# Optimization experiments

Hardware: AMD Instinct MI355X
Metric: run time of the kernel (lower is better)

## Reference

```python
import jax, jax.numpy as jnp
import numpy as np

N = 10000       # n_nodes
E = 640000      # n_edges (avg degree 64)
D_IN = 128      # in_feats
D_H = 128       # n_hidden
N_CLS = 64      # n_classes


def setup_inputs() -> dict:
    key = jax.random.key(0)
    k1, k2, k3, k4, k5, k6 = jax.random.split(key, 6)
    features = jax.random.normal(k1, (N, D_IN), dtype=jnp.float32)
    src = jax.random.randint(k2, (E,), 0, N, dtype=jnp.int32)
    dst = jax.random.randint(k3, (E,), 0, N, dtype=jnp.int32)
    s = 0.05  # small init scale to keep activations bounded across 3 layers
    # Stored as [in, out]; equivalent to torch Linear weight [out, in] transposed.
    W0 = jax.random.normal(k4, (D_IN, D_H), dtype=jnp.float32) * s
    W1 = jax.random.normal(k5, (D_H, D_H), dtype=jnp.float32) * s
    W2 = jax.random.normal(k6, (D_H, N_CLS), dtype=jnp.float32) * s
    return {"features": features, "W0": W0, "W1": W1, "W2": W2,
            "src": src, "dst": dst}


def reference(features, W0, W1, W2, src, dst):
    # GINConv with aggregator 'sum', eps=0 (learn_eps=False):
    #   h' = Linear(h + sum_{(u->v) in E} h[u] scattered to v)
    # Dropout is identity at inference; 'activation' is unused in the module.
    def gin_layer(h, W):
        agg = jax.ops.segment_sum(h[src], dst, num_segments=N)  # [N, d]
        return (h + agg) @ W

    h = gin_layer(features, W0)
    h = gin_layer(h, W1)
    h = gin_layer(h, W2)
    return h
```

## Files before the change

kernel.cpp:

```cpp
#include <hip/hip_runtime.h>
#include <hip/hip_bf16.h>

#define NN 10000
#define NE 640000
#define D_IN 128
#define D_H 128
#define N_CLS 64
#define CAP 160
#define GRP 157
#define CAPC 4800
#define CCS 16
#define SENT 10000
#define EPB 1024
#define AB 625
#define W01B 16
#define WPB 4

__device__ __forceinline__ float blo(unsigned u) { return __uint_as_float(u << 16); }
__device__ __forceinline__ float bhi(unsigned u) { return __uint_as_float(u & 0xffff0000u); }
__device__ __forceinline__ unsigned short f2bf(float f) {
    unsigned u = __float_as_uint(f);
    return (unsigned short)((u + 0x7fffu + ((u >> 16) & 1u)) >> 16);
}
__device__ __forceinline__ unsigned packbf(float a, float b) {
    return (unsigned)f2bf(a) | ((unsigned)f2bf(b) << 16);
}

__global__ __launch_bounds__(256) void prep_a(const int* __restrict__ src,
                                              const int* __restrict__ dst,
                                              int* __restrict__ coarse_cnt,
                                              unsigned* __restrict__ coarse,
                                              const float* __restrict__ W0,
                                              const float* __restrict__ W1,
                                              float* __restrict__ W01) {
    int bid = blockIdx.x;
    if (bid >= AB) {
        int t = (bid - AB) * 256 + threadIdx.x;
        int i = t >> 5;
        int jb = (t & 31) << 2;
        float c0 = 0.f, c1 = 0.f, c2 = 0.f, c3 = 0.f;
        for (int k = 0; k < 128; ++k) {
            float a = W0[i * 128 + k];
            float4 b = *(const float4*)&W1[k * 128 + jb];
            c0 += a * b.x; c1 += a * b.y; c2 += a * b.z; c3 += a * b.w;
        }
        *(float4*)&W01[i * 128 + jb] = make_float4(c0, c1, c2, c3);
        return;
    }
    __shared__ unsigned stage[EPB];
    __shared__ int hist[GRP], gbase[GRP], cur[GRP];
    const int t = threadIdx.x;
    for (int i = t; i < GRP; i += 256) hist[i] = 0;
    __syncthreads();
    const int e0 = bid * EPB;
    for (int i = t; i < EPB; i += 256) {
        int s = src[e0 + i];
        int d = dst[e0 + i];
        stage[i] = (unsigned)s | ((unsigned)d << 16);
        atomicAdd(&hist[d >> 6], 1);
    }
    __syncthreads();
    for (int i = t; i < GRP; i += 256) {
        gbase[i] = atomicAdd(&coarse_cnt[i * CCS], hist[i]);
        cur[i] = 0;
    }
    __syncthreads();
    for (int i = t; i < EPB; i += 256) {
        unsigned u = stage[i];
        int g = u >> 22;
        int r = atomicAdd(&cur[g], 1);
        coarse[g * CAPC + gbase[g] + r] = u;
    }
}

__global__ __launch_bounds__(1024) void prep_b(const int* __restrict__ coarse_cnt,
                                               const unsigned* __restrict__ coarse,
                                               int* __restrict__ cnt,
                                               unsigned short* __restrict__ colbuf,
                                               const float* __restrict__ W01,
                                               const float* __restrict__ W2,
                                               unsigned* __restrict__ wbp) {
    const int g = blockIdx.x;
    const int t = threadIdx.x;
    if (g >= GRP) {
        int s = (g - GRP) * 1024 + t;
        int kp = s >> 6, j = s & 63;
        float c0 = 0.f, c1 = 0.f;
        const float* r0 = W01 + (2 * kp) * 128;
        const float* r1 = r0 + 128;
        for (int k = 0; k < 128; ++k) {
            float w2 = W2[k * 64 + j];
            c0 += r0[k] * w2;
            c1 += r1[k] * w2;
        }
        wbp[kp * 64 + j] = packbf(c0, c1);
        return;
    }
    __shared__ int cur[64];
    __shared__ unsigned short sbuf[64][CAP];
    if (t < 64) cur[t] = 0;
    __syncthreads();
    const int m = coarse_cnt[g * CCS];
    const unsigned* cb = coarse + g * CAPC;
    for (int i = t; i < m; i += 1024) {
        unsigned u = cb[i];
        int s = (int)(u & 0xFFFFu);
        int dl = (int)(u >> 16) - (g << 6);
        int r = atomicAdd(&cur[dl], 1);
        sbuf[dl][r] = (unsigned short)s;
    }
    __syncthreads();
    if (t < 64) {
        int n = (g << 6) + t;
        if (n < NN) {
            int c = cur[t];
            int pad = (32 - (c & 31)) & 31;
            for (int k = 0; k < pad; ++k) sbuf[t][c + k] = (unsigned short)SENT;
            cnt[n] = c + pad;
        }
    }
    __syncthreads();
    const uint4* s4 = (const uint4*)sbuf;
    for (int idx = t; idx < 64 * (CAP / 8); idx += 1024) {
        int node = (g << 6) + (idx / (CAP / 8));
        if (node < NN)
            ((uint4*)colbuf)[(size_t)node * (CAP / 8) + (idx % (CAP / 8))] = s4[idx];
    }
}

__global__ __launch_bounds__(256, 4) void gemm0(const float* __restrict__ feat,
                                                const unsigned* __restrict__ Wbp,
                                                unsigned short* __restrict__ g0) {
    __shared__ float xs[4][128];
    const int tid = threadIdx.x;
    const int wave = tid >> 6;
    const int lane = tid & 63;
    const int n = blockIdx.x * 4 + wave;
    float2 f = *(const float2*)&feat[(size_t)n * 128 + lane * 2];
    xs[wave][lane * 2]     = f.x;
    xs[wave][lane * 2 + 1] = f.y;
    __syncthreads();
    const int j = lane;
    float acc = 0.f;
    for (int k = 0; k < 128; k += 4) {
        unsigned wp0 = Wbp[(k >> 1) * 64 + j];
        unsigned wp1 = Wbp[((k >> 1) + 1) * 64 + j];
        float4 xv = *(const float4*)&xs[wave][k];
        acc += xv.x * blo(wp0) + xv.y * bhi(wp0) + xv.z * blo(wp1) + xv.w * bhi(wp1);
    }
    g0[(size_t)n * 64 + j] = f2bf(acc);
    if (blockIdx.x == 0 && tid < 16) {
        ((uint2*)(g0 + (size_t)SENT * 64))[tid] = make_uint2(0u, 0u);
    }
}

__global__ __launch_bounds__(256, 4) void agg64b(const uint4* __restrict__ tb4,
                                                 const int* __restrict__ cnt,
                                                 const unsigned short* __restrict__ colbuf,
                                                 unsigned short* __restrict__ tb2) {
    constexpr int M = 4;
    const int base = blockIdx.x * M;
    const int tid = threadIdx.x;
    const int wave = tid >> 6;
    const int lane = tid & 63;
    const int sub = lane >> 3;
    const int off = lane & 7;

    const int n = __builtin_amdgcn_readfirstlane(base + wave);
    float a0, a1, a2, a3, a4, a5, a6, a7;
    if (sub == 0) {
        uint4 u = tb4[n * 8 + off];
        a0 = blo(u.x); a1 = bhi(u.x); a2 = blo(u.y); a3 = bhi(u.y);
        a4 = blo(u.z); a5 = bhi(u.z); a6 = blo(u.w); a7 = bhi(u.w);
    } else {
        a0 = a1 = a2 = a3 = a4 = a5 = a6 = a7 = 0.f;
    }
    const int NCH = __builtin_amdgcn_readfirstlane(cnt[n]) >> 5;
    const uint2* cl = (const uint2*)(colbuf + n * CAP);
    const int hi4 = sub >> 2;
    const int wsel = (sub >> 1) & 1;
    const int sh = (sub & 1) << 4;
    uint2 p0 = cl[0], p1 = cl[1], p2 = cl[2], p3 = cl[3];
    uint2 p4 = cl[4], p5 = cl[5], p6 = cl[6], p7 = cl[7];
    for (int c = 0; c < NCH; ++c) {
        unsigned q0 = hi4 ? (wsel ? p1.y : p1.x) : (wsel ? p0.y : p0.x);
        unsigned q1 = hi4 ? (wsel ? p3.y : p3.x) : (wsel ? p2.y : p2.x);
        unsigned q2 = hi4 ? (wsel ? p5.y : p5.x) : (wsel ? p4.y : p4.x);
        unsigned q3 = hi4 ? (wsel ? p7.y : p7.x) : (wsel ? p6.y : p6.x);
        int s0 = (int)((q0 >> sh) & 0xffffu);
        int s1 = (int)((q1 >> sh) & 0xffffu);
        int s2 = (int)((q2 >> sh) & 0xffffu);
        int s3 = (int)((q3 >> sh) & 0xffffu);
        uint4 u0 = tb4[s0 * 8 + off];
        uint4 u1 = tb4[s1 * 8 + off];
        uint4 u2 = tb4[s2 * 8 + off];
        uint4 u3 = tb4[s3 * 8 + off];
        {
            const uint2* nx = cl + 8 * (c + 1);
            p0 = nx[0]; p1 = nx[1]; p2 = nx[2]; p3 = nx[3];
            p4 = nx[4]; p5 = nx[5]; p6 = nx[6]; p7 = nx[7];
        }
        a0 += (blo(u0.x) + blo(u1.x)) + (blo(u2.x) + blo(u3.x));
        a1 += (bhi(u0.x) + bhi(u1.x)) + (bhi(u2.x) + bhi(u3.x));
        a2 += (blo(u0.y) + blo(u1.y)) + (blo(u2.y) + blo(u3.y));
        a3 += (bhi(u0.y) + bhi(u1.y)) + (bhi(u2.y) + bhi(u3.y));
        a4 += (blo(u0.z) + blo(u1.z)) + (blo(u2.z) + blo(u3.z));
        a5 += (bhi(u0.z) + bhi(u1.z)) + (bhi(u2.z) + bhi(u3.z));
        a6 += (blo(u0.w) + blo(u1.w)) + (blo(u2.w) + blo(u3.w));
        a7 += (bhi(u0.w) + bhi(u1.w)) + (bhi(u2.w) + bhi(u3.w));
    }
    a0 += __shfl_xor(a0, 8); a0 += __shfl_xor(a0, 16); a0 += __shfl_xor(a0, 32);
    a1 += __shfl_xor(a1, 8); a1 += __shfl_xor(a1, 16); a1 += __shfl_xor(a1, 32);
    a2 += __shfl_xor(a2, 8); a2 += __shfl_xor(a2, 16); a2 += __shfl_xor(a2, 32);
    a3 += __shfl_xor(a3, 8); a3 += __shfl_xor(a3, 16); a3 += __shfl_xor(a3, 32);
    a4 += __shfl_xor(a4, 8); a4 += __shfl_xor(a4, 16); a4 += __shfl_xor(a4, 32);
    a5 += __shfl_xor(a5, 8); a5 += __shfl_xor(a5, 16); a5 += __shfl_xor(a5, 32);
    a6 += __shfl_xor(a6, 8); a6 += __shfl_xor(a6, 16); a6 += __shfl_xor(a6, 32);
    a7 += __shfl_xor(a7, 8); a7 += __shfl_xor(a7, 16); a7 += __shfl_xor(a7, 32);
    if (sub == 0) {
        unsigned short* o = tb2 + (size_t)n * 64 + 8 * off;
        *(uint4*)o = make_uint4(packbf(a0, a1), packbf(a2, a3),
                                packbf(a4, a5), packbf(a6, a7));
    }
    if (blockIdx.x == 0 && tid < 16) {
        ((uint2*)(tb2 + (size_t)SENT * 64))[tid] = make_uint2(0u, 0u);
    }
}

__global__ __launch_bounds__(256, 4) void agg64f(const uint4* __restrict__ tb4,
                                                 const int* __restrict__ cnt,
                                                 const unsigned short* __restrict__ colbuf,
                                                 float* __restrict__ outf) {
    constexpr int M = 4;
    const int base = blockIdx.x * M;
    const int tid = threadIdx.x;
    const int wave = tid >> 6;
    const int lane = tid & 63;
    const int sub = lane >> 3;
    const int off = lane & 7;

    const int n = __builtin_amdgcn_readfirstlane(base + wave);
    float a0, a1, a2, a3, a4, a5, a6, a7;
    if (sub == 0) {
        uint4 u = tb4[n * 8 + off];
        a0 = blo(u.x); a1 = bhi(u.x); a2 = blo(u.y); a3 = bhi(u.y);
        a4 = blo(u.z); a5 = bhi(u.z); a6 = blo(u.w); a7 = bhi(u.w);
    } else {
        a0 = a1 = a2 = a3 = a4 = a5 = a6 = a7 = 0.f;
    }
    const int NCH = __builtin_amdgcn_readfirstlane(cnt[n]) >> 5;
    const uint2* cl = (const uint2*)(colbuf + n * CAP);
    const int hi4 = sub >> 2;
    const int wsel = (sub >> 1) & 1;
    const int sh = (sub & 1) << 4;
    uint2 p0 = cl[0], p1 = cl[1], p2 = cl[2], p3 = cl[3];
    uint2 p4 = cl[4], p5 = cl[5], p6 = cl[6], p7 = cl[7];
    for (int c = 0; c < NCH; ++c) {
        unsigned q0 = hi4 ? (wsel ? p1.y : p1.x) : (wsel ? p0.y : p0.x);
        unsigned q1 = hi4 ? (wsel ? p3.y : p3.x) : (wsel ? p2.y : p2.x);
        unsigned q2 = hi4 ? (wsel ? p5.y : p5.x) : (wsel ? p4.y : p4.x);
        unsigned q3 = hi4 ? (wsel ? p7.y : p7.x) : (wsel ? p6.y : p6.x);
        int s0 = (int)((q0 >> sh) & 0xffffu);
        int s1 = (int)((q1 >> sh) & 0xffffu);
        int s2 = (int)((q2 >> sh) & 0xffffu);
        int s3 = (int)((q3 >> sh) & 0xffffu);
        uint4 u0 = tb4[s0 * 8 + off];
        uint4 u1 = tb4[s1 * 8 + off];
        uint4 u2 = tb4[s2 * 8 + off];
        uint4 u3 = tb4[s3 * 8 + off];
        {
            const uint2* nx = cl + 8 * (c + 1);
            p0 = nx[0]; p1 = nx[1]; p2 = nx[2]; p3 = nx[3];
            p4 = nx[4]; p5 = nx[5]; p6 = nx[6]; p7 = nx[7];
        }
        a0 += (blo(u0.x) + blo(u1.x)) + (blo(u2.x) + blo(u3.x));
        a1 += (bhi(u0.x) + bhi(u1.x)) + (bhi(u2.x) + bhi(u3.x));
        a2 += (blo(u0.y) + blo(u1.y)) + (blo(u2.y) + blo(u3.y));
        a3 += (bhi(u0.y) + bhi(u1.y)) + (bhi(u2.y) + bhi(u3.y));
        a4 += (blo(u0.z) + blo(u1.z)) + (blo(u2.z) + blo(u3.z));
        a5 += (bhi(u0.z) + bhi(u1.z)) + (bhi(u2.z) + bhi(u3.z));
        a6 += (blo(u0.w) + blo(u1.w)) + (blo(u2.w) + blo(u3.w));
        a7 += (bhi(u0.w) + bhi(u1.w)) + (bhi(u2.w) + bhi(u3.w));
    }
    a0 += __shfl_xor(a0, 8); a0 += __shfl_xor(a0, 16); a0 += __shfl_xor(a0, 32);
    a1 += __shfl_xor(a1, 8); a1 += __shfl_xor(a1, 16); a1 += __shfl_xor(a1, 32);
    a2 += __shfl_xor(a2, 8); a2 += __shfl_xor(a2, 16); a2 += __shfl_xor(a2, 32);
    a3 += __shfl_xor(a3, 8); a3 += __shfl_xor(a3, 16); a3 += __shfl_xor(a3, 32);
    a4 += __shfl_xor(a4, 8); a4 += __shfl_xor(a4, 16); a4 += __shfl_xor(a4, 32);
    a5 += __shfl_xor(a5, 8); a5 += __shfl_xor(a5, 16); a5 += __shfl_xor(a5, 32);
    a6 += __shfl_xor(a6, 8); a6 += __shfl_xor(a6, 16); a6 += __shfl_xor(a6, 32);
    a7 += __shfl_xor(a7, 8); a7 += __shfl_xor(a7, 16); a7 += __shfl_xor(a7, 32);
    if (sub == 0) {
        float* o = outf + (size_t)n * N_CLS + 8 * off;
        *(float4*)o       = make_float4(a0, a1, a2, a3);
        *(float4*)(o + 4) = make_float4(a4, a5, a6, a7);
    }
}

extern "C" void kernel_launch(void* const* d_in, const int* in_sizes, int n_in,
                              void* d_out, int out_size, void* d_ws, size_t ws_size,
                              hipStream_t stream) {
    const float* feat = (const float*)d_in[0];
    const float* W0   = (const float*)d_in[1];
    const float* W1   = (const float*)d_in[2];
    const float* W2   = (const float*)d_in[3];
    const int*   src  = (const int*)d_in[4];
    const int*   dst  = (const int*)d_in[5];
    float* out = (float*)d_out;

    int* coarse_cnt        = (int*)d_ws;
    int* cnt               = coarse_cnt + GRP * CCS;
    unsigned short* colbuf = (unsigned short*)(cnt + NN + 8);
    unsigned* coarse       = (unsigned*)(colbuf + (size_t)NN * CAP);
    unsigned* g0u          = coarse + (size_t)GRP * CAPC;
    unsigned* tbu          = g0u + (size_t)(NN + 1) * 32;
    unsigned* tb2u         = tbu + (size_t)(NN + 1) * 32;
    float* W01             = (float*)(tb2u + (size_t)(NN + 1) * 32);
    unsigned* wbp          = (unsigned*)(W01 + 16384);
    unsigned short* g0     = (unsigned short*)g0u;
    unsigned short* tb     = (unsigned short*)tbu;
    unsigned short* tb2    = (unsigned short*)tb2u;

    hipMemsetAsync(coarse_cnt, 0, GRP * CCS * sizeof(int), stream);
    prep_a<<<AB + W01B, 256, 0, stream>>>(src, dst, coarse_cnt, coarse, W0, W1, W01);
    prep_b<<<GRP + WPB, 1024, 0, stream>>>(coarse_cnt, coarse, cnt, colbuf,
                                           W01, W2, wbp);

    gemm0<<<NN / 4, 256, 0, stream>>>(feat, wbp, g0);
    agg64b<<<NN / 4, 256, 0, stream>>>((const uint4*)g0, cnt, colbuf, tb);
    agg64b<<<NN / 4, 256, 0, stream>>>((const uint4*)tb, cnt, colbuf, tb2);
    agg64f<<<NN / 4, 256, 0, stream>>>((const uint4*)tb2, cnt, colbuf, out);
}
```

Measured before the change: 137.2 us.

## Build CSR adjacency with direct global atomics instead of two-level bucketing

Replaces the two-pass coarse-bucket then shared-memory fine-sort construction of per-node neighbor lists with a single pass that does global atomicAdd on per-node counters and scatters 16-bit source indices directly into colbuf, followed by a light padding kernel. This removes the intermediate coarse buffer and a large shared-memory kernel, but adds 640k contended global atomics and scattered 2-byte writes. It also makes neighbor order within a row nondeterministic, which changes the floating-point summation order.

```diff
diff --git a/kernel.cpp b/kernel.cpp
--- a/kernel.cpp
+++ b/kernel.cpp
@@ -7,14 +7,11 @@
 #define D_H 128
 #define N_CLS 64
 #define CAP 160
-#define GRP 157
-#define CAPC 4800
-#define CCS 16
 #define SENT 10000
-#define EPB 1024
-#define AB 625
+#define EB 625
 #define W01B 16
-#define WPB 4
+#define PB 40
+#define WPB 16
 
 __device__ __forceinline__ float blo(unsigned u) { return __uint_as_float(u << 16); }
 __device__ __forceinline__ float bhi(unsigned u) { return __uint_as_float(u & 0xffff0000u); }
@@ -26,16 +23,16 @@
     return (unsigned)f2bf(a) | ((unsigned)f2bf(b) << 16);
 }
 
-__global__ __launch_bounds__(256) void prep_a(const int* __restrict__ src,
-                                              const int* __restrict__ dst,
-                                              int* __restrict__ coarse_cnt,
-                                              unsigned* __restrict__ coarse,
-                                              const float* __restrict__ W0,
-                                              const float* __restrict__ W1,
-                                              float* __restrict__ W01) {
+__global__ __launch_bounds__(256) void prep1(const int* __restrict__ src,
+                                             const int* __restrict__ dst,
+                                             int* __restrict__ cnt,
+                                             unsigned short* __restrict__ colbuf,
+                                             const float* __restrict__ W0,
+                                             const float* __restrict__ W1,
+                                             float* __restrict__ W01) {
     int bid = blockIdx.x;
-    if (bid >= AB) {
-        int t = (bid - AB) * 256 + threadIdx.x;
+    if (bid >= EB) {
+        int t = (bid - EB) * 256 + threadIdx.x;
         int i = t >> 5;
         int jb = (t & 31) << 2;
         float c0 = 0.f, c1 = 0.f, c2 = 0.f, c3 = 0.f;
@@ -47,43 +44,24 @@
         *(float4*)&W01[i * 128 + jb] = make_float4(c0, c1, c2, c3);
         return;
     }
-    __shared__ unsigned stage[EPB];
-    __shared__ int hist[GRP], gbase[GRP], cur[GRP];
-    const int t = threadIdx.x;
-    for (int i = t; i < GRP; i += 256) hist[i] = 0;
-    __syncthreads();
-    const int e0 = bid * EPB;
-    for (int i = t; i < EPB; i += 256) {
-        int s = src[e0 + i];
-        int d = dst[e0 + i];
-        stage[i] = (unsigned)s | ((unsigned)d << 16);
-        atomicAdd(&hist[d >> 6], 1);
-    }
-    __syncthreads();
-    for (int i = t; i < GRP; i += 256) {
-        gbase[i] = atomicAdd(&coarse_cnt[i * CCS], hist[i]);
-        cur[i] = 0;
-    }
-    __syncthreads();
-    for (int i = t; i < EPB; i += 256) {
-        unsigned u = stage[i];
-        int g = u >> 22;
-        int r = atomicAdd(&cur[g], 1);
-        coarse[g * CAPC + gbase[g] + r] = u;
-    }
-}
-
-__global__ __launch_bounds__(1024) void prep_b(const int* __restrict__ coarse_cnt,
-                                               const unsigned* __restrict__ coarse,
-                                               int* __restrict__ cnt,
-                                               unsigned short* __restrict__ colbuf,
-                                               const float* __restrict__ W01,
-                                               const float* __restrict__ W2,
-                                               unsigned* __restrict__ wbp) {
-    const int g = blockIdx.x;
-    const int t = threadIdx.x;
-    if (g >= GRP) {
-        int s = (g - GRP) * 1024 + t;
+    int t = bid * 256 + threadIdx.x;
+    int4 s4 = ((const int4*)src)[t];
+    int4 d4 = ((const int4*)dst)[t];
+    int r;
+    r = atomicAdd(&cnt[d4.x], 1); colbuf[(size_t)d4.x * CAP + r] = (unsigned short)s4.x;
+    r = atomicAdd(&cnt[d4.y], 1); colbuf[(size_t)d4.y * CAP + r] = (unsigned short)s4.y;
+    r = atomicAdd(&cnt[d4.z], 1); colbuf[(size_t)d4.z * CAP + r] = (unsigned short)s4.z;
+    r = atomicAdd(&cnt[d4.w], 1); colbuf[(size_t)d4.w * CAP + r] = (unsigned short)s4.w;
+}
+
+__global__ __launch_bounds__(256) void prep2(int* __restrict__ cnt,
+                                             unsigned short* __restrict__ colbuf,
+                                             const float* __restrict__ W01,
+                                             const float* __restrict__ W2,
+                                             unsigned* __restrict__ wbp) {
+    int bid = blockIdx.x;
+    if (bid >= PB) {
+        int s = (bid - PB) * 256 + threadIdx.x;
         int kp = s >> 6, j = s & 63;
         float c0 = 0.f, c1 = 0.f;
         const float* r0 = W01 + (2 * kp) * 128;
@@ -96,35 +74,13 @@
         wbp[kp * 64 + j] = packbf(c0, c1);
         return;
     }
-    __shared__ int cur[64];
-    __shared__ unsigned short sbuf[64][CAP];
-    if (t < 64) cur[t] = 0;
-    __syncthreads();
-    const int m = coarse_cnt[g * CCS];
-    const unsigned* cb = coarse + g * CAPC;
-    for (int i = t; i < m; i += 1024) {
-        unsigned u = cb[i];
-        int s = (int)(u & 0xFFFFu);
-        int dl = (int)(u >> 16) - (g << 6);
-        int r = atomicAdd(&cur[dl], 1);
-        sbuf[dl][r] = (unsigned short)s;
-    }
-    __syncthreads();
-    if (t < 64) {
-        int n = (g << 6) + t;
-        if (n < NN) {
-            int c = cur[t];
-            int pad = (32 - (c & 31)) & 31;
-            for (int k = 0; k < pad; ++k) sbuf[t][c + k] = (unsigned short)SENT;
-            cnt[n] = c + pad;
-        }
-    }
-    __syncthreads();
-    const uint4* s4 = (const uint4*)sbuf;
-    for (int idx = t; idx < 64 * (CAP / 8); idx += 1024) {
-        int node = (g << 6) + (idx / (CAP / 8));
-        if (node < NN)
-            ((uint4*)colbuf)[(size_t)node * (CAP / 8) + (idx % (CAP / 8))] = s4[idx];
+    int n = bid * 256 + threadIdx.x;
+    if (n < NN) {
+        int c = cnt[n];
+        int pad = (32 - (c & 31)) & 31;
+        unsigned short* b = colbuf + (size_t)n * CAP;
+        for (int k = 0; k < pad; ++k) b[c + k] = (unsigned short)SENT;
+        cnt[n] = c + pad;
     }
 }
 
@@ -176,7 +132,7 @@
         a0 = a1 = a2 = a3 = a4 = a5 = a6 = a7 = 0.f;
     }
     const int NCH = __builtin_amdgcn_readfirstlane(cnt[n]) >> 5;
-    const uint2* cl = (const uint2*)(colbuf + n * CAP);
+    const uint2* cl = (const uint2*)(colbuf + (size_t)n * CAP);
     const int hi4 = sub >> 2;
     const int wsel = (sub >> 1) & 1;
     const int sh = (sub & 1) << 4;
@@ -249,7 +205,7 @@
         a0 = a1 = a2 = a3 = a4 = a5 = a6 = a7 = 0.f;
     }
     const int NCH = __builtin_amdgcn_readfirstlane(cnt[n]) >> 5;
-    const uint2* cl = (const uint2*)(colbuf + n * CAP);
+    const uint2* cl = (const uint2*)(colbuf + (size_t)n * CAP);
     const int hi4 = sub >> 2;
     const int wsel = (sub >> 1) & 1;
     const int sh = (sub & 1) << 4;
@@ -308,11 +264,9 @@
     const int*   dst  = (const int*)d_in[5];
     float* out = (float*)d_out;
 
-    int* coarse_cnt        = (int*)d_ws;
-    int* cnt               = coarse_cnt + GRP * CCS;
-    unsigned short* colbuf = (unsigned short*)(cnt + NN + 8);
-    unsigned* coarse       = (unsigned*)(colbuf + (size_t)NN * CAP);
-    unsigned* g0u          = coarse + (size_t)GRP * CAPC;
+    int* cnt               = (int*)d_ws;
+    unsigned short* colbuf = (unsigned short*)(cnt + NN + 32);
+    unsigned* g0u          = (unsigned*)(colbuf + (size_t)NN * CAP + 64);
     unsigned* tbu          = g0u + (size_t)(NN + 1) * 32;
     unsigned* tb2u         = tbu + (size_t)(NN + 1) * 32;
     float* W01             = (float*)(tb2u + (size_t)(NN + 1) * 32);
@@ -321,10 +275,9 @@
     unsigned short* tb     = (unsigned short*)tbu;
     unsigned short* tb2    = (unsigned short*)tb2u;
 
-    hipMemsetAsync(coarse_cnt, 0, GRP * CCS * sizeof(int), stream);
-    prep_a<<<AB + W01B, 256, 0, stream>>>(src, dst, coarse_cnt, coarse, W0, W1, W01);
-    prep_b<<<GRP + WPB, 1024, 0, stream>>>(coarse_cnt, coarse, cnt, colbuf,
-                                           W01, W2, wbp);
+    (void)hipMemsetAsync(cnt, 0, NN * sizeof(int), stream);
+    prep1<<<EB + W01B, 256, 0, stream>>>(src, dst, cnt, colbuf, W0, W1, W01);
+    prep2<<<PB + WPB, 256, 0, stream>>>(cnt, colbuf, W01, W2, wbp);
 
     gemm0<<<NN / 4, 256, 0, stream>>>(feat, wbp, g0);
     agg64b<<<NN / 4, 256, 0, stream>>>((const uint4*)g0, cnt, colbuf, tb);
```

Result: slower. 152.9 us (+11.4%).

## Fuse gemm and three aggregation passes into one cooperative persistent kernel

Applied to the files above, without the earlier changes.

Replaces the four separate launches (gemm0 and three aggregation passes) with a single cooperative kernel on a fixed grid of 1024 blocks. Each block loops over node blocks and uses grid-wide syncs between stages. The aim is to remove kernel launch gaps and tail effects between dependent stages. In exchange it adds grid barrier cost and ties concurrency to the fixed grid size. It falls back to the old launches if the cooperative launch fails.

```diff
diff --git a/kernel.cpp b/kernel.cpp
--- a/kernel.cpp
+++ b/kernel.cpp
@@ -1,5 +1,8 @@
 #include <hip/hip_runtime.h>
 #include <hip/hip_bf16.h>
+#include <hip/hip_cooperative_groups.h>
+
+namespace cg = cooperative_groups;
 
 #define NN 10000
 #define NE 640000
@@ -15,6 +18,8 @@
 #define AB 625
 #define W01B 16
 #define WPB 4
+#define CGRID 1024
+#define NBLK (NN / 4)
 
 __device__ __forceinline__ float blo(unsigned u) { return __uint_as_float(u << 16); }
 __device__ __forceinline__ float bhi(unsigned u) { return __uint_as_float(u & 0xffff0000u); }
@@ -128,55 +133,44 @@
     }
 }
 
-__global__ __launch_bounds__(256, 4) void gemm0(const float* __restrict__ feat,
-                                                const unsigned* __restrict__ Wbp,
-                                                unsigned short* __restrict__ g0) {
-    __shared__ float xs[4][128];
-    const int tid = threadIdx.x;
-    const int wave = tid >> 6;
-    const int lane = tid & 63;
-    const int n = blockIdx.x * 4 + wave;
+__device__ __forceinline__ void gemm0_step(const float* __restrict__ feat,
+                                           const unsigned* __restrict__ Wbp,
+                                           unsigned short* __restrict__ g0,
+                                           float xsrow[128],
+                                           int n, int lane) {
     float2 f = *(const float2*)&feat[(size_t)n * 128 + lane * 2];
-    xs[wave][lane * 2]     = f.x;
-    xs[wave][lane * 2 + 1] = f.y;
-    __syncthreads();
-    const int j = lane;
+    xsrow[lane * 2]     = f.x;
+    xsrow[lane * 2 + 1] = f.y;
     float acc = 0.f;
     for (int k = 0; k < 128; k += 4) {
-        unsigned wp0 = Wbp[(k >> 1) * 64 + j];
-        unsigned wp1 = Wbp[((k >> 1) + 1) * 64 + j];
-        float4 xv = *(const float4*)&xs[wave][k];
+        unsigned wp0 = Wbp[(k >> 1) * 64 + lane];
+        unsigned wp1 = Wbp[((k >> 1) + 1) * 64 + lane];
+        float4 xv = *(const float4*)&xsrow[k];
         acc += xv.x * blo(wp0) + xv.y * bhi(wp0) + xv.z * blo(wp1) + xv.w * bhi(wp1);
     }
-    g0[(size_t)n * 64 + j] = f2bf(acc);
-    if (blockIdx.x == 0 && tid < 16) {
-        ((uint2*)(g0 + (size_t)SENT * 64))[tid] = make_uint2(0u, 0u);
-    }
-}
-
-__global__ __launch_bounds__(256, 4) void agg64b(const uint4* __restrict__ tb4,
-                                                 const int* __restrict__ cnt,
-                                                 const unsigned short* __restrict__ colbuf,
-                                                 unsigned short* __restrict__ tb2) {
-    constexpr int M = 4;
-    const int base = blockIdx.x * M;
-    const int tid = threadIdx.x;
-    const int wave = tid >> 6;
-    const int lane = tid & 63;
+    g0[(size_t)n * 64 + lane] = f2bf(acc);
+}
+
+template <bool LAST>
+__device__ __forceinline__ void agg_step(const uint4* __restrict__ in4,
+                                         const int* __restrict__ cnt,
+                                         const unsigned short* __restrict__ colbuf,
+                                         unsigned short* __restrict__ outb,
+                                         float* __restrict__ outf,
+                                         int blk, int wave, int lane) {
     const int sub = lane >> 3;
     const int off = lane & 7;
-
-    const int n = __builtin_amdgcn_readfirstlane(base + wave);
+    const int n = __builtin_amdgcn_readfirstlane(blk * 4 + wave);
     float a0, a1, a2, a3, a4, a5, a6, a7;
     if (sub == 0) {
-        uint4 u = tb4[n * 8 + off];
+        uint4 u = in4[n * 8 + off];
         a0 = blo(u.x); a1 = bhi(u.x); a2 = blo(u.y); a3 = bhi(u.y);
         a4 = blo(u.z); a5 = bhi(u.z); a6 = blo(u.w); a7 = bhi(u.w);
     } else {
         a0 = a1 = a2 = a3 = a4 = a5 = a6 = a7 = 0.f;
     }
     const int NCH = __builtin_amdgcn_readfirstlane(cnt[n]) >> 5;
-    const uint2* cl = (const uint2*)(colbuf + n * CAP);
+    const uint2* cl = (const uint2*)(colbuf + (size_t)n * CAP);
     const int hi4 = sub >> 2;
     const int wsel = (sub >> 1) & 1;
     const int sh = (sub & 1) << 4;
@@ -191,10 +185,10 @@
         int s1 = (int)((q1 >> sh) & 0xffffu);
         int s2 = (int)((q2 >> sh) & 0xffffu);
         int s3 = (int)((q3 >> sh) & 0xffffu);
-        uint4 u0 = tb4[s0 * 8 + off];
-        uint4 u1 = tb4[s1 * 8 + off];
-        uint4 u2 = tb4[s2 * 8 + off];
-        uint4 u3 = tb4[s3 * 8 + off];
+        uint4 u0 = in4[s0 * 8 + off];
+        uint4 u1 = in4[s1 * 8 + off];
+        uint4 u2 = in4[s2 * 8 + off];
+        uint4 u3 = in4[s3 * 8 + off];
         {
             const uint2* nx = cl + 8 * (c + 1);
             p0 = nx[0]; p1 = nx[1]; p2 = nx[2]; p3 = nx[3];
@@ -218,10 +212,37 @@
     a6 += __shfl_xor(a6, 8); a6 += __shfl_xor(a6, 16); a6 += __shfl_xor(a6, 32);
     a7 += __shfl_xor(a7, 8); a7 += __shfl_xor(a7, 16); a7 += __shfl_xor(a7, 32);
     if (sub == 0) {
-        unsigned short* o = tb2 + (size_t)n * 64 + 8 * off;
-        *(uint4*)o = make_uint4(packbf(a0, a1), packbf(a2, a3),
-                                packbf(a4, a5), packbf(a6, a7));
-    }
+        if (LAST) {
+            float* o = outf + (size_t)n * N_CLS + 8 * off;
+            *(float4*)o       = make_float4(a0, a1, a2, a3);
+            *(float4*)(o + 4) = make_float4(a4, a5, a6, a7);
+        } else {
+            unsigned short* o = outb + (size_t)n * 64 + 8 * off;
+            *(uint4*)o = make_uint4(packbf(a0, a1), packbf(a2, a3),
+                                    packbf(a4, a5), packbf(a6, a7));
+        }
+    }
+}
+
+__global__ __launch_bounds__(256, 4) void gemm0(const float* __restrict__ feat,
+                                                const unsigned* __restrict__ Wbp,
+                                                unsigned short* __restrict__ g0) {
+    __shared__ float xs[4][128];
+    const int tid = threadIdx.x;
+    const int wave = tid >> 6;
+    const int lane = tid & 63;
+    gemm0_step(feat, Wbp, g0, xs[wave], blockIdx.x * 4 + wave, lane);
+    if (blockIdx.x == 0 && tid < 16) {
+        ((uint2*)(g0 + (size_t)SENT * 64))[tid] = make_uint2(0u, 0u);
+    }
+}
+
+__global__ __launch_bounds__(256, 4) void agg64b(const uint4* __restrict__ tb4,
+                                                 const int* __restrict__ cnt,
+                                                 const unsigned short* __restrict__ colbuf,
+                                                 unsigned short* __restrict__ tb2) {
+    const int tid = threadIdx.x;
+    agg_step<false>(tb4, cnt, colbuf, tb2, nullptr, blockIdx.x, tid >> 6, tid & 63);
     if (blockIdx.x == 0 && tid < 16) {
         ((uint2*)(tb2 + (size_t)SENT * 64))[tid] = make_uint2(0u, 0u);
     }
@@ -231,70 +252,44 @@
                                                  const int* __restrict__ cnt,
                                                  const unsigned short* __restrict__ colbuf,
                                                  float* __restrict__ outf) {
-    constexpr int M = 4;
-    const int base = blockIdx.x * M;
+    const int tid = threadIdx.x;
+    agg_step<true>(tb4, cnt, colbuf, nullptr, outf, blockIdx.x, tid >> 6, tid & 63);
+}
+
+__global__ __launch_bounds__(256, 4) void mega(const float* __restrict__ feat,
+                                               const unsigned* __restrict__ Wbp,
+                                               unsigned short* __restrict__ g0,
+                                               const int* __restrict__ cnt,
+                                               const unsigned short* __restrict__ colbuf,
+                                               unsigned short* __restrict__ tb,
+                                               unsigned short* __restrict__ tb2,
+                                               float* __restrict__ outf) {
+    cg::grid_group grid = cg::this_grid();
+    __shared__ float xs[4][128];
     const int tid = threadIdx.x;
     const int wave = tid >> 6;
     const int lane = tid & 63;
-    const int sub = lane >> 3;
-    const int off = lane & 7;
-
-    const int n = __builtin_amdgcn_readfirstlane(base + wave);
-    float a0, a1, a2, a3, a4, a5, a6, a7;
-    if (sub == 0) {
-        uint4 u = tb4[n * 8 + off];
-        a0 = blo(u.x); a1 = bhi(u.x); a2 = blo(u.y); a3 = bhi(u.y);
-        a4 = blo(u.z); a5 = bhi(u.z); a6 = blo(u.w); a7 = bhi(u.w);
-    } else {
-        a0 = a1 = a2 = a3 = a4 = a5 = a6 = a7 = 0.f;
-    }
-    const int NCH = __builtin_amdgcn_readfirstlane(cnt[n]) >> 5;
-    const uint2* cl = (const uint2*)(colbuf + n * CAP);
-    const int hi4 = sub >> 2;
-    const int wsel = (sub >> 1) & 1;
-    const int sh = (sub & 1) << 4;
-    uint2 p0 = cl[0], p1 = cl[1], p2 = cl[2], p3 = cl[3];
-    uint2 p4 = cl[4], p5 = cl[5], p6 = cl[6], p7 = cl[7];
-    for (int c = 0; c < NCH; ++c) {
-        unsigned q0 = hi4 ? (wsel ? p1.y : p1.x) : (wsel ? p0.y : p0.x);
-        unsigned q1 = hi4 ? (wsel ? p3.y : p3.x) : (wsel ? p2.y : p2.x);
-        unsigned q2 = hi4 ? (wsel ? p5.y : p5.x) : (wsel ? p4.y : p4.x);
-        unsigned q3 = hi4 ? (wsel ? p7.y : p7.x) : (wsel ? p6.y : p6.x);
-        int s0 = (int)((q0 >> sh) & 0xffffu);
-        int s1 = (int)((q1 >> sh) & 0xffffu);
-        int s2 = (int)((q2 >> sh) & 0xffffu);
-        int s3 = (int)((q3 >> sh) & 0xffffu);
-        uint4 u0 = tb4[s0 * 8 + off];
-        uint4 u1 = tb4[s1 * 8 + off];
-        uint4 u2 = tb4[s2 * 8 + off];
-        uint4 u3 = tb4[s3 * 8 + off];
-        {
-            const uint2* nx = cl + 8 * (c + 1);
-            p0 = nx[0]; p1 = nx[1]; p2 = nx[2]; p3 = nx[3];
-            p4 = nx[4]; p5 = nx[5]; p6 = nx[6]; p7 = nx[7];
-        }
-        a0 += (blo(u0.x) + blo(u1.x)) + (blo(u2.x) + blo(u3.x));
-        a1 += (bhi(u0.x) + bhi(u1.x)) + (bhi(u2.x) + bhi(u3.x));
-        a2 += (blo(u0.y) + blo(u1.y)) + (blo(u2.y) + blo(u3.y));
-        a3 += (bhi(u0.y) + bhi(u1.y)) + (bhi(u2.y) + bhi(u3.y));
-        a4 += (blo(u0.z) + blo(u1.z)) + (blo(u2.z) + blo(u3.z));
-        a5 += (bhi(u0.z) + bhi(u1.z)) + (bhi(u2.z) + bhi(u3.z));
-        a6 += (blo(u0.w) + blo(u1.w)) + (blo(u2.w) + blo(u3.w));
-        a7 += (bhi(u0.w) + bhi(u1.w)) + (bhi(u2.w) + bhi(u3.w));
-    }
-    a0 += __shfl_xor(a0, 8); a0 += __shfl_xor(a0, 16); a0 += __shfl_xor(a0, 32);
-    a1 += __shfl_xor(a1, 8); a1 += __shfl_xor(a1, 16); a1 += __shfl_xor(a1, 32);
-    a2 += __shfl_xor(a2, 8); a2 += __shfl_xor(a2, 16); a2 += __shfl_xor(a2, 32);
-    a3 += __shfl_xor(a3, 8); a3 += __shfl_xor(a3, 16); a3 += __shfl_xor(a3, 32);
-    a4 += __shfl_xor(a4, 8); a4 += __shfl_xor(a4, 16); a4 += __shfl_xor(a4, 32);
-    a5 += __shfl_xor(a5, 8); a5 += __shfl_xor(a5, 16); a5 += __shfl_xor(a5, 32);
-    a6 += __shfl_xor(a6, 8); a6 += __shfl_xor(a6, 16); a6 += __shfl_xor(a6, 32);
-    a7 += __shfl_xor(a7, 8); a7 += __shfl_xor(a7, 16); a7 += __shfl_xor(a7, 32);
-    if (sub == 0) {
-        float* o = outf + (size_t)n * N_CLS + 8 * off;
-        *(float4*)o       = make_float4(a0, a1, a2, a3);
-        *(float4*)(o + 4) = make_float4(a4, a5, a6, a7);
-    }
+
+    for (int blk = blockIdx.x; blk < NBLK; blk += CGRID)
+        gemm0_step(feat, Wbp, g0, xs[wave], blk * 4 + wave, lane);
+    if (blockIdx.x == 0 && tid < 16)
+        ((uint2*)(g0 + (size_t)SENT * 64))[tid] = make_uint2(0u, 0u);
+    grid.sync();
+
+    for (int blk = blockIdx.x; blk < NBLK; blk += CGRID)
+        agg_step<false>((const uint4*)g0, cnt, colbuf, tb, nullptr, blk, wave, lane);
+    if (blockIdx.x == 0 && tid < 16)
+        ((uint2*)(tb + (size_t)SENT * 64))[tid] = make_uint2(0u, 0u);
+    grid.sync();
+
+    for (int blk = blockIdx.x; blk < NBLK; blk += CGRID)
+        agg_step<false>((const uint4*)tb, cnt, colbuf, tb2, nullptr, blk, wave, lane);
+    if (blockIdx.x == 0 && tid < 16)
+        ((uint2*)(tb2 + (size_t)SENT * 64))[tid] = make_uint2(0u, 0u);
+    grid.sync();
+
+    for (int blk = blockIdx.x; blk < NBLK; blk += CGRID)
+        agg_step<true>((const uint4*)tb2, cnt, colbuf, nullptr, outf, blk, wave, lane);
 }
 
 extern "C" void kernel_launch(void* const* d_in, const int* in_sizes, int n_in,
@@ -321,13 +316,27 @@
     unsigned short* tb     = (unsigned short*)tbu;
     unsigned short* tb2    = (unsigned short*)tb2u;
 
-    hipMemsetAsync(coarse_cnt, 0, GRP * CCS * sizeof(int), stream);
+    (void)hipMemsetAsync(coarse_cnt, 0, GRP * CCS * sizeof(int), stream);
     prep_a<<<AB + W01B, 256, 0, stream>>>(src, dst, coarse_cnt, coarse, W0, W1, W01);
     prep_b<<<GRP + WPB, 1024, 0, stream>>>(coarse_cnt, coarse, cnt, colbuf,
                                            W01, W2, wbp);
 
-    gemm0<<<NN / 4, 256, 0, stream>>>(feat, wbp, g0);
-    agg64b<<<NN / 4, 256, 0, stream>>>((const uint4*)g0, cnt, colbuf, tb);
-    agg64b<<<NN / 4, 256, 0, stream>>>((const uint4*)tb, cnt, colbuf, tb2);
-    agg64f<<<NN / 4, 256, 0, stream>>>((const uint4*)tb2, cnt, colbuf, out);
-}
+    const float* feat_ = feat;
+    const unsigned* wbp_ = wbp;
+    unsigned short* g0_ = g0;
+    const int* cnt_ = cnt;
+    const unsigned short* colbuf_ = colbuf;
+    unsigned short* tb_ = tb;
+    unsigned short* tb2_ = tb2;
+    float* out_ = out;
+    void* kargs[] = {(void*)&feat_, (void*)&wbp_, (void*)&g0_, (void*)&cnt_,
+                     (void*)&colbuf_, (void*)&tb_, (void*)&tb2_, (void*)&out_};
+    hipError_t ce = hipLaunchCooperativeKernel((void*)mega, dim3(CGRID), dim3(256),
+                                               kargs, 0, stream);
+    if (ce != hipSuccess) {
+        gemm0<<<NBLK, 256, 0, stream>>>(feat, wbp, g0);
+        agg64b<<<NBLK, 256, 0, stream>>>((const uint4*)g0, cnt, colbuf, tb);
+        agg64b<<<NBLK, 256, 0, stream>>>((const uint4*)tb, cnt, colbuf, tb2);
+        agg64f<<<NBLK, 256, 0, stream>>>((const uint4*)tb2, cnt, colbuf, out);
+    }
+}
```

New measurement: 538.0 us. +292.2%, slower.
